# Kernel optimization log

Measured on AMD Instinct MI355X. Metric: run time of the kernel, lower is better.

Reference implementation:

```python
import jax, jax.numpy as jnp
import numpy as np

DIM = 512
HID = 1024
E = 8          # num_experts
K = 2          # num_experts_per_tok
B, S = 4, 2048


def setup_inputs() -> dict:
    key = jax.random.key(0)
    ks = jax.random.split(key, 10)
    sd = DIM ** -0.5
    sh = HID ** -0.5
    return {
        "x": jax.random.normal(ks[0], (B, S, DIM), dtype=jnp.float32),
        "gate_w": jax.random.normal(ks[1], (E, DIM), dtype=jnp.float32) * sd,
        "biases": jnp.zeros((E,), dtype=jnp.float32),  # e_expert_biases
        # routed experts: swiglu  y = (silu(x@w1) * (x@w3)) @ w2
        "w1": jax.random.normal(ks[2], (E, DIM, HID), dtype=jnp.float32) * sd,
        "w3": jax.random.normal(ks[3], (E, DIM, HID), dtype=jnp.float32) * sd,
        "w2": jax.random.normal(ks[4], (E, HID, DIM), dtype=jnp.float32) * sh,
        # single shared expert
        "sw1": jax.random.normal(ks[5], (DIM, HID), dtype=jnp.float32) * sd,
        "sw3": jax.random.normal(ks[6], (DIM, HID), dtype=jnp.float32) * sd,
        "sw2": jax.random.normal(ks[7], (HID, DIM), dtype=jnp.float32) * sh,
    }


def reference(x, gate_w, biases, w1, w3, w2, sw1, sw3, sw2):
    Bb, Ss, D = x.shape
    xt = x.reshape(Bb * Ss, D)                      # [T, D]

    # shared expert (applied to full x)
    shared = (jax.nn.silu(xt @ sw1) * (xt @ sw3)) @ sw2  # [T, D]

    # router
    scores = xt @ gate_w.T                          # [T, E]
    # indices chosen from biased scores (aux-free load balancing)
    _, idx = jax.lax.top_k(scores + biases, K)      # [T, K] int
    # gate values are top-k of the UNBIASED scores (as in original code)
    topv, _ = jax.lax.top_k(scores, K)              # [T, K]
    p = jax.nn.sigmoid(topv)
    p = p / jnp.sum(p, axis=-1, keepdims=True)      # [T, K]

    # every expert on every token (dense-combine MoE reference)
    h = jax.nn.silu(jnp.einsum('td,edh->eth', xt, w1)) * jnp.einsum('td,edh->eth', xt, w3)
    y = jnp.einsum('eth,ehd->etd', h, w2)           # [E, T, D]

    onehot = jax.nn.one_hot(idx, E, dtype=xt.dtype)  # [T, K, E]
    comb = jnp.einsum('tk,tke->te', p, onehot)       # [T, E] combine weights
    out = jnp.einsum('te,etd->td', comb, y) + shared
    return out.reshape(Bb, Ss, D)
```

## Files before the change

kernel.cpp:

```cpp
#include <hip/hip_runtime.h>
#include <hip/hip_bf16.h>


#define Tn 8192
#define Dd 512
#define Hh 1024
#define NEx 9

typedef __attribute__((ext_vector_type(8))) short short8;
typedef __attribute__((ext_vector_type(4))) float f32x4;

#define AS1 __attribute__((address_space(1)))
#define AS3 __attribute__((address_space(3)))

#define OFF_XB    ((size_t)0)
#define OFF_W13T  (OFF_XB + (size_t)Tn * Dd * 2)
#define OFF_W2T   (OFF_W13T + (size_t)NEx * 2 * Hh * Dd * 2)
#define OFF_HBUF  (OFF_W2T + (size_t)NEx * Dd * Hh * 2)
#define OFF_TOK   (OFF_HBUF + (size_t)(3 * Tn) * Hh * 2)
#define OFF_SLOTP (OFF_TOK + (size_t)8 * Tn * 4)
#define OFF_PG    (OFF_SLOTP + (size_t)Tn * 2 * 4)
#define OFF_CNT   (OFF_PG + (size_t)Tn * 2 * 4)
#define OFF_OFFS  (OFF_CNT + 1024)
#define OFF_YC    OFF_XB

__device__ __forceinline__ ushort f2bf(float f) {
    unsigned int u = __float_as_uint(f);
    return (ushort)((u + 0x7fffu + ((u >> 16) & 1u)) >> 16);
}
__device__ __forceinline__ float bf2f(short s) {
    return __uint_as_float(((unsigned int)(unsigned short)s) << 16);
}

__global__ __launch_bounds__(256) void trans_kernel(
        const float* __restrict__ w1, const float* __restrict__ sw1,
        const float* __restrict__ w3, const float* __restrict__ sw3,
        const float* __restrict__ w2, const float* __restrict__ sw2,
        ushort* __restrict__ w13t, ushort* __restrict__ w2t) {
    __shared__ float tile[32][33];
    int z = blockIdx.z;
    int fam = z / 9, sl = z - fam * 9;
    int tx = threadIdx.x & 31, ty = threadIdx.x >> 5;
    if (fam < 2) {
        const float* base = (fam == 0) ? ((sl < 8) ? w1 + (size_t)sl * Dd * Hh : sw1)
                                       : ((sl < 8) ? w3 + (size_t)sl * Dd * Hh : sw3);
        ushort* dst = w13t + (size_t)sl * 2 * Hh * Dd;
        int c0 = blockIdx.x * 32, r0 = blockIdx.y * 32;
#pragma unroll
        for (int k = 0; k < 4; ++k)
            tile[ty + 8 * k][tx] = base[(size_t)(r0 + ty + 8 * k) * Hh + c0 + tx];
        __syncthreads();
#pragma unroll
        for (int k = 0; k < 4; ++k) {
            int h = c0 + ty + 8 * k;
            int n = (((h >> 4) * 2 + fam) << 4) + (h & 15);
            dst[(size_t)n * Dd + r0 + tx] = f2bf(tile[tx][ty + 8 * k]);
        }
    } else {
        const float* base = (sl < 8) ? w2 + (size_t)sl * Dd * Hh : sw2;
        ushort* dst = w2t + (size_t)sl * Dd * Hh;
        int r0 = blockIdx.x * 32, c0 = blockIdx.y * 32;
#pragma unroll
        for (int k = 0; k < 4; ++k)
            tile[ty + 8 * k][tx] = base[(size_t)(r0 + ty + 8 * k) * Dd + c0 + tx];
        __syncthreads();
#pragma unroll
        for (int k = 0; k < 4; ++k)
            dst[(size_t)(c0 + ty + 8 * k) * Hh + r0 + tx] = f2bf(tile[tx][ty + 8 * k]);
    }
}

__global__ __launch_bounds__(256) void router_kernel(const float* __restrict__ x,
                                                     const float* __restrict__ gw,
                                                     const float* __restrict__ bias,
                                                     int* __restrict__ cnt,
                                                     int* __restrict__ tok,
                                                     int* __restrict__ slotp,
                                                     float* __restrict__ pg,
                                                     ushort* __restrict__ xb) {
    __shared__ int le[64];
    __shared__ float lg[64];
    __shared__ int lpos[64];
    __shared__ int lcnt[8];
    __shared__ int gbase[8];
    int tid = threadIdx.x, lane = tid & 63, wave = tid >> 6;
    if (tid < 8) lcnt[tid] = 0;
    __syncthreads();
    int t0 = blockIdx.x * 32 + wave * 8;
    for (int it = 0; it < 8; ++it) {
        int t = t0 + it;
        const float4* xr = (const float4*)(x + (size_t)t * Dd);
        float4 xa = xr[lane * 2], xc = xr[lane * 2 + 1];
        ushort4 o1, o2;
        o1.x = f2bf(xa.x); o1.y = f2bf(xa.y); o1.z = f2bf(xa.z); o1.w = f2bf(xa.w);
        o2.x = f2bf(xc.x); o2.y = f2bf(xc.y); o2.z = f2bf(xc.z); o2.w = f2bf(xc.w);
        *(ushort4*)(xb + (size_t)t * Dd + lane * 8) = o1;
        *(ushort4*)(xb + (size_t)t * Dd + lane * 8 + 4) = o2;
        float sc[8];
#pragma unroll
        for (int e = 0; e < 8; ++e) {
            const float4* gr = (const float4*)(gw + (size_t)e * Dd);
            float4 ga = gr[lane * 2], gc = gr[lane * 2 + 1];
            float s = xa.x * ga.x + xa.y * ga.y + xa.z * ga.z + xa.w * ga.w
                    + xc.x * gc.x + xc.y * gc.y + xc.z * gc.z + xc.w * gc.w;
#pragma unroll
            for (int o = 32; o > 0; o >>= 1) s += __shfl_xor(s, o);
            sc[e] = s;
        }
        if (lane == 0) {
            float b0 = -1e30f; int i0 = 0;
#pragma unroll
            for (int e = 0; e < 8; ++e) { float bv = sc[e] + bias[e]; if (bv > b0) { b0 = bv; i0 = e; } }
            float b1v = -1e30f; int i1 = (i0 == 0) ? 1 : 0;
#pragma unroll
            for (int e = 0; e < 8; ++e) if (e != i0) { float bv = sc[e] + bias[e]; if (bv > b1v) { b1v = bv; i1 = e; } }
            float v0 = -1e30f; int k0i = 0;
#pragma unroll
            for (int e = 0; e < 8; ++e) if (sc[e] > v0) { v0 = sc[e]; k0i = e; }
            float v1 = -1e30f;
#pragma unroll
            for (int e = 0; e < 8; ++e) if (e != k0i && sc[e] > v1) v1 = sc[e];
            float p0 = 1.f / (1.f + __expf(-v0));
            float p1 = 1.f / (1.f + __expf(-v1));
            float inv = 1.f / (p0 + p1);
            int ai = (wave * 8 + it) * 2;
            le[ai] = i0;     lg[ai] = p0 * inv;
            le[ai + 1] = i1; lg[ai + 1] = p1 * inv;
        }
    }
    __syncthreads();
    if (tid < 64) lpos[tid] = atomicAdd(&lcnt[le[tid]], 1);
    __syncthreads();
    if (tid < 8) gbase[tid] = atomicAdd(&cnt[tid * 32], lcnt[tid]);
    __syncthreads();
    if (tid < 64) {
        int e = le[tid];
        int dst = gbase[e] + lpos[tid];
        int t = blockIdx.x * 32 + (tid >> 1);
        tok[(size_t)e * Tn + dst] = t;
        slotp[t * 2 + (tid & 1)] = (e << 16) | dst;
        pg[t * 2 + (tid & 1)] = lg[tid];
    }
}

__global__ void scan_kernel(const int* cnt, int* off, int* cntc) {
    if (threadIdx.x == 0 && blockIdx.x == 0) {
        int s = 0;
        for (int e = 0; e < 8; ++e) { int c = cnt[e * 32]; cntc[e] = c; off[e] = s; s += c; }
        off[8] = s;
        cntc[8] = Tn;
    }
}

__global__ __launch_bounds__(256, 2) void stage1_kernel(
        const ushort* __restrict__ xb, const ushort* __restrict__ w13t,
        const int* __restrict__ tok, const int* __restrict__ cntc,
        const int* __restrict__ off, ushort* __restrict__ Hbuf) {
    int e = blockIdx.z;
    int cn = cntc[e];
    int m0 = blockIdx.x * 128;
    if (m0 >= cn) return;
    int n0 = blockIdx.y * 128;
    const ushort* we = w13t + (size_t)e * 2 * Hh * Dd;

    __shared__ ushort As[128 * 64];
    __shared__ ushort Bs[128 * 64];
    __shared__ int toks[128];

    int tid = threadIdx.x;
    if (tid < 128) {
        int slot = m0 + tid;
        int sl = slot < cn ? slot : cn - 1;
        toks[tid] = (e == 8) ? sl : tok[(size_t)e * Tn + sl];
    }
    __syncthreads();

    int lane = tid & 63, wave = tid >> 6;
    int wm = (wave & 1) * 64, wn = (wave >> 1) * 64;
    int col15 = lane & 15, quad = lane >> 4;
    int lr = lane >> 3;
    int lcx = ((lane & 7) ^ lr) * 8;

    f32x4 acc[4][4];
#pragma unroll
    for (int a = 0; a < 4; ++a)
#pragma unroll
        for (int b = 0; b < 4; ++b) acc[a][b] = (f32x4){0.f, 0.f, 0.f, 0.f};

    for (int kb = 0; kb < Dd; kb += 64) {
#pragma unroll
        for (int i = 0; i < 4; ++i) {
            int cid = wave * 4 + i;
            const ushort* g = xb + (size_t)toks[cid * 8 + lr] * Dd + kb + lcx;
            __builtin_amdgcn_global_load_lds((const AS1 void*)g, (AS3 void*)(As + cid * 512), 16, 0, 0);
        }
#pragma unroll
        for (int i = 0; i < 4; ++i) {
            int cid = wave * 4 + i;
            const ushort* g = we + (size_t)(n0 + cid * 8 + lr) * Dd + kb + lcx;
            __builtin_amdgcn_global_load_lds((const AS1 void*)g, (AS3 void*)(Bs + cid * 512), 16, 0, 0);
        }
        __syncthreads();
#pragma unroll
        for (int ks = 0; ks < 2; ++ks) {
            int px = ((ks * 4 + quad) ^ (col15 & 7)) * 8;
            short8 a[4], b[4];
#pragma unroll
            for (int mi = 0; mi < 4; ++mi)
                a[mi] = *(const short8*)&As[(wm + mi * 16 + col15) * 64 + px];
#pragma unroll
            for (int ni = 0; ni < 4; ++ni)
                b[ni] = *(const short8*)&Bs[(wn + ni * 16 + col15) * 64 + px];
#pragma unroll
            for (int mi = 0; mi < 4; ++mi)
#pragma unroll
                for (int ni = 0; ni < 4; ++ni)
                    acc[mi][ni] = __builtin_amdgcn_mfma_f32_16x16x32_bf16(a[mi], b[ni], acc[mi][ni], 0, 0, 0);
        }
        __syncthreads();
    }

    int oe = off[e];
    int hbase = (n0 + wn) >> 1;
#pragma unroll
    for (int mi = 0; mi < 4; ++mi)
#pragma unroll
        for (int r = 0; r < 4; ++r) {
            int slot = m0 + wm + mi * 16 + quad * 4 + r;
            if (slot < cn) {
                size_t rowb = (size_t)(oe + slot) * Hh;
#pragma unroll
                for (int np = 0; np < 2; ++np) {
                    float h1 = acc[mi][np * 2][r], h3 = acc[mi][np * 2 + 1][r];
                    float s = h1 / (1.f + __expf(-h1));
                    Hbuf[rowb + hbase + np * 16 + col15] = f2bf(s * h3);
                }
            }
        }
}

__global__ __launch_bounds__(256, 3) void stage2_kernel(
        const ushort* __restrict__ Hbuf, const ushort* __restrict__ w2t,
        const int* __restrict__ cntc, const int* __restrict__ off,
        ushort* __restrict__ Yc) {
    int e = blockIdx.z;
    int cn = cntc[e];
    int m0 = blockIdx.x * 128;
    if (m0 >= cn) return;
    int n0 = blockIdx.y * 128;
    int oe = off[e];
    const ushort* w2e = w2t + (size_t)e * Dd * Hh;

    __shared__ ushort As[128 * 64];
    __shared__ ushort Bs[128 * 64];

    int tid = threadIdx.x;
    int lane = tid & 63, wave = tid >> 6;
    int wm = (wave & 1) * 64, wn = (wave >> 1) * 64;
    int col15 = lane & 15, quad = lane >> 4;
    int lr = lane >> 3;
    int lcx = ((lane & 7) ^ lr) * 8;

    f32x4 acc[4][4];
#pragma unroll
    for (int a = 0; a < 4; ++a)
#pragma unroll
        for (int b = 0; b < 4; ++b) acc[a][b] = (f32x4){0.f, 0.f, 0.f, 0.f};

    for (int kb = 0; kb < Hh; kb += 64) {
#pragma unroll
        for (int i = 0; i < 4; ++i) {
            int cid = wave * 4 + i;
            const ushort* g = Hbuf + (size_t)(oe + m0 + cid * 8 + lr) * Hh + kb + lcx;
            __builtin_amdgcn_global_load_lds((const AS1 void*)g, (AS3 void*)(As + cid * 512), 16, 0, 0);
        }
#pragma unroll
        for (int i = 0; i < 4; ++i) {
            int cid = wave * 4 + i;
            const ushort* g = w2e + (size_t)(n0 + cid * 8 + lr) * Hh + kb + lcx;
            __builtin_amdgcn_global_load_lds((const AS1 void*)g, (AS3 void*)(Bs + cid * 512), 16, 0, 0);
        }
        __syncthreads();
#pragma unroll
        for (int ks = 0; ks < 2; ++ks) {
            int px = ((ks * 4 + quad) ^ (col15 & 7)) * 8;
            short8 a[4], b[4];
#pragma unroll
            for (int mi = 0; mi < 4; ++mi)
                a[mi] = *(const short8*)&As[(wm + mi * 16 + col15) * 64 + px];
#pragma unroll
            for (int ni = 0; ni < 4; ++ni)
                b[ni] = *(const short8*)&Bs[(wn + ni * 16 + col15) * 64 + px];
#pragma unroll
            for (int mi = 0; mi < 4; ++mi)
#pragma unroll
                for (int ni = 0; ni < 4; ++ni)
                    acc[mi][ni] = __builtin_amdgcn_mfma_f32_16x16x32_bf16(a[mi], b[ni], acc[mi][ni], 0, 0, 0);
        }
        __syncthreads();
    }

#pragma unroll
    for (int mi = 0; mi < 4; ++mi)
#pragma unroll
        for (int r = 0; r < 4; ++r) {
            int slot = m0 + wm + mi * 16 + quad * 4 + r;
            if (slot < cn) {
                size_t rowb = (size_t)(oe + slot) * Dd;
#pragma unroll
                for (int ni = 0; ni < 4; ++ni)
                    Yc[rowb + n0 + wn + ni * 16 + col15] = f2bf(acc[mi][ni][r]);
            }
        }
}

__global__ __launch_bounds__(256) void combine_kernel(const ushort* __restrict__ Yc,
        const int* __restrict__ slotp, const float* __restrict__ pg,
        const int* __restrict__ off, float* __restrict__ out) {
    int g = blockIdx.x * 256 + threadIdx.x;
    int t = g >> 6;
    int c = (g & 63) * 8;
    int p0 = slotp[t * 2], p1 = slotp[t * 2 + 1];
    float g0 = pg[t * 2], g1 = pg[t * 2 + 1];
    int s0 = off[p0 >> 16] + (p0 & 0xffff);
    int s1 = off[p1 >> 16] + (p1 & 0xffff);
    int s2 = off[8] + t;
    short8 a = *(const short8*)(Yc + (size_t)s0 * Dd + c);
    short8 b = *(const short8*)(Yc + (size_t)s1 * Dd + c);
    short8 d = *(const short8*)(Yc + (size_t)s2 * Dd + c);
    float o[8];
#pragma unroll
    for (int i = 0; i < 8; ++i)
        o[i] = g0 * bf2f(a[i]) + g1 * bf2f(b[i]) + bf2f(d[i]);
    float* dst = out + (size_t)t * Dd + c;
    *(float4*)dst = (float4){o[0], o[1], o[2], o[3]};
    *(float4*)(dst + 4) = (float4){o[4], o[5], o[6], o[7]};
}

extern "C" void kernel_launch(void* const* d_in, const int* in_sizes, int n_in,
                              void* d_out, int out_size, void* d_ws, size_t ws_size,
                              hipStream_t stream) {
    (void)in_sizes; (void)n_in; (void)out_size; (void)ws_size;
    const float* x    = (const float*)d_in[0];
    const float* gw   = (const float*)d_in[1];
    const float* bias = (const float*)d_in[2];
    const float* w1   = (const float*)d_in[3];
    const float* w3   = (const float*)d_in[4];
    const float* w2   = (const float*)d_in[5];
    const float* sw1  = (const float*)d_in[6];
    const float* sw3  = (const float*)d_in[7];
    const float* sw2  = (const float*)d_in[8];
    float* out = (float*)d_out;

    char* ws = (char*)d_ws;
    ushort* xb    = (ushort*)(ws + OFF_XB);
    ushort* w13t  = (ushort*)(ws + OFF_W13T);
    ushort* w2t   = (ushort*)(ws + OFF_W2T);
    ushort* Hbuf  = (ushort*)(ws + OFF_HBUF);
    ushort* Yc    = (ushort*)(ws + OFF_YC);
    int*    tok   = (int*)(ws + OFF_TOK);
    int*    slotp = (int*)(ws + OFF_SLOTP);
    float*  pg    = (float*)(ws + OFF_PG);
    int*    cnt   = (int*)(ws + OFF_CNT);
    int*    off   = (int*)(ws + OFF_OFFS);
    int*    cntc  = off + 16;

    hipMemsetAsync(cnt, 0, 1024, stream);

    trans_kernel<<<dim3(32, 16, 27), 256, 0, stream>>>(w1, sw1, w3, sw3, w2, sw2, w13t, w2t);
    router_kernel<<<256, 256, 0, stream>>>(x, gw, bias, cnt, tok, slotp, pg, xb);
    scan_kernel<<<1, 64, 0, stream>>>(cnt, off, cntc);

    stage1_kernel<<<dim3(64, 16, NEx), 256, 0, stream>>>(xb, w13t, tok, cntc, off, Hbuf);
    stage2_kernel<<<dim3(64, Dd / 128, NEx), 256, 0, stream>>>(Hbuf, w2t, cntc, off, Yc);
    combine_kernel<<<2048, 256, 0, stream>>>(Yc, slotp, pg, off, out);
}
```

Before: 264.1 us.

## Use 256x256 tiles with 8 waves and double-buffered ping-pong LDS pipeline

Replaces the 128x128, 4-wave grouped GEMM tiles in both expert stages with a shared 256x256 core using 8 waves and 128 KB of LDS in two stages. Async global-to-LDS loads are interleaved with MFMA quarter-blocks under explicit barriers, waitcnts and setprio. The goal is more data reuse per tile and hiding global load latency behind compute. In exchange, the larger tiles waste more work on partial expert tiles and launch fewer blocks, which could hurt occupancy and load balance.

```diff
diff --git a/kernel.cpp b/kernel.cpp
--- a/kernel.cpp
+++ b/kernel.cpp
@@ -152,81 +152,157 @@
     }
 }
 
-__global__ __launch_bounds__(256, 2) void stage1_kernel(
+__device__ __forceinline__ void mm256_core(
+        const ushort* (&aSrc)[2][2], const ushort* (&bSrc)[2][2],
+        ushort* smem, int KK, f32x4 (&acc)[8][4]) {
+    const int tid = threadIdx.x;
+    const int lane = tid & 63, wid = tid >> 6;
+    const int wm = wid >> 2, wn = wid & 3, hb = wn >> 1, wn1 = wn & 1;
+    const int col15 = lane & 15, quad = lane >> 4, sw7 = col15 & 7;
+
+    ushort* Ard = smem + wm * 8192;
+    ushort* Brd = smem + 32768 + hb * 8192;
+    ushort* Adst = smem + wid * 1024;
+    ushort* Bdst = smem + 32768 + wid * 1024;
+
+    auto rdA = [&](int s, int mi, int ks) -> short8 {
+        return *(const short8*)&Ard[s * 16384 + mi * 1024 + col15 * 64 + (((ks * 4 + quad) ^ sw7) << 3)];
+    };
+    auto rdB = [&](int s, int ni, int ks) -> short8 {
+        return *(const short8*)&Brd[s * 16384 + (wn1 * 64 + ni * 16 + col15) * 64 + (((ks * 4 + quad) ^ sw7) << 3)];
+    };
+    auto stA = [&](int s, int h, int kb) {
+        if (kb < KK) {
+            __builtin_amdgcn_global_load_lds((const AS1 void*)(aSrc[h][0] + kb), (AS3 void*)(Adst + (s * 2 + h) * 8192), 16, 0, 0);
+            __builtin_amdgcn_global_load_lds((const AS1 void*)(aSrc[h][1] + kb), (AS3 void*)(Adst + (s * 2 + h) * 8192 + 512), 16, 0, 0);
+        }
+    };
+    auto stB = [&](int s, int h, int kb) {
+        if (kb < KK) {
+            __builtin_amdgcn_global_load_lds((const AS1 void*)(bSrc[h][0] + kb), (AS3 void*)(Bdst + (s * 2 + h) * 8192), 16, 0, 0);
+            __builtin_amdgcn_global_load_lds((const AS1 void*)(bSrc[h][1] + kb), (AS3 void*)(Bdst + (s * 2 + h) * 8192 + 512), 16, 0, 0);
+        }
+    };
+
+    short8 aF[4][2], bF0[2][2], bF1[2][2];
+    auto ldA = [&](int s, int mh) {
+#pragma unroll
+        for (int j = 0; j < 4; ++j) { aF[j][0] = rdA(s, mh * 4 + j, 0); aF[j][1] = rdA(s, mh * 4 + j, 1); }
+    };
+    auto ldB = [&](int s, int nh, short8 (&bF)[2][2]) {
+#pragma unroll
+        for (int t = 0; t < 2; ++t) { bF[t][0] = rdB(s, nh * 2 + t, 0); bF[t][1] = rdB(s, nh * 2 + t, 1); }
+    };
+    auto mmq = [&](int mh, int nh, short8 (&bF)[2][2]) {
+        __builtin_amdgcn_s_setprio(1);
+#pragma unroll
+        for (int j = 0; j < 4; ++j)
+#pragma unroll
+            for (int t = 0; t < 2; ++t) {
+                acc[mh * 4 + j][nh * 2 + t] = __builtin_amdgcn_mfma_f32_16x16x32_bf16(aF[j][0], bF[t][0], acc[mh * 4 + j][nh * 2 + t], 0, 0, 0);
+                acc[mh * 4 + j][nh * 2 + t] = __builtin_amdgcn_mfma_f32_16x16x32_bf16(aF[j][1], bF[t][1], acc[mh * 4 + j][nh * 2 + t], 0, 0, 0);
+            }
+        __builtin_amdgcn_s_setprio(0);
+    };
+
+#define BAR()  __builtin_amdgcn_s_barrier()
+#define LGK0() do { asm volatile("s_waitcnt lgkmcnt(0)" ::: "memory"); __builtin_amdgcn_sched_barrier(0); } while (0)
+
+    stA(0, 0, 0); stB(0, 0, 0); stB(0, 1, 0); stA(0, 1, 0);
+    stA(1, 0, 64); stB(1, 0, 64);
+    asm volatile("s_waitcnt vmcnt(4)" ::: "memory");
+    BAR();
+
+    const int NIT = KK >> 7;
+    for (int i = 0; i < NIT; ++i) {
+        const int k0 = i << 7;
+        const bool tail = (i == NIT - 1);
+        ldA(0, 0); ldB(0, 0, bF0);
+        stA(1, 1, k0 + 64);
+        BAR(); LGK0(); mmq(0, 0, bF0); BAR();
+        ldB(0, 1, bF1);
+        stB(1, 1, k0 + 64);
+        BAR(); LGK0(); mmq(0, 1, bF1); BAR();
+        ldA(0, 1);
+        stA(0, 0, k0 + 128);
+        BAR(); LGK0(); mmq(1, 0, bF0); BAR();
+        stB(0, 0, k0 + 128);
+        BAR(); mmq(1, 1, bF1);
+        if (tail) asm volatile("s_waitcnt vmcnt(0)" ::: "memory");
+        else      asm volatile("s_waitcnt vmcnt(4)" ::: "memory");
+        BAR();
+        ldA(1, 0); ldB(1, 0, bF0);
+        stB(0, 1, k0 + 128);
+        BAR(); LGK0(); mmq(0, 0, bF0); BAR();
+        ldB(1, 1, bF1);
+        stA(0, 1, k0 + 128);
+        BAR(); LGK0(); mmq(0, 1, bF1); BAR();
+        ldA(1, 1);
+        stA(1, 0, k0 + 192);
+        BAR(); LGK0(); mmq(1, 0, bF0); BAR();
+        stB(1, 0, k0 + 192);
+        BAR(); mmq(1, 1, bF1);
+        if (tail) asm volatile("s_waitcnt vmcnt(0)" ::: "memory");
+        else      asm volatile("s_waitcnt vmcnt(4)" ::: "memory");
+        BAR();
+    }
+#undef BAR
+#undef LGK0
+}
+
+__global__ __launch_bounds__(512, 2) void stage1_kernel(
         const ushort* __restrict__ xb, const ushort* __restrict__ w13t,
         const int* __restrict__ tok, const int* __restrict__ cntc,
         const int* __restrict__ off, ushort* __restrict__ Hbuf) {
+    __shared__ __align__(16) ushort smem[65536];
+    __shared__ int toks[256];
     int e = blockIdx.z;
     int cn = cntc[e];
-    int m0 = blockIdx.x * 128;
+    int m0 = blockIdx.x * 256;
     if (m0 >= cn) return;
-    int n0 = blockIdx.y * 128;
+    int n0 = blockIdx.y * 256;
     const ushort* we = w13t + (size_t)e * 2 * Hh * Dd;
 
-    __shared__ ushort As[128 * 64];
-    __shared__ ushort Bs[128 * 64];
-    __shared__ int toks[128];
-
     int tid = threadIdx.x;
-    if (tid < 128) {
+    if (tid < 256) {
         int slot = m0 + tid;
         int sl = slot < cn ? slot : cn - 1;
         toks[tid] = (e == 8) ? sl : tok[(size_t)e * Tn + sl];
     }
     __syncthreads();
 
-    int lane = tid & 63, wave = tid >> 6;
-    int wm = (wave & 1) * 64, wn = (wave >> 1) * 64;
+    int lane = tid & 63, wid = tid >> 6;
+    int lr = lane >> 3, l7 = lane & 7;
+    int lcx = (l7 ^ lr) << 3;
+
+    const ushort* aSrc[2][2];
+    const ushort* bSrc[2][2];
+#pragma unroll
+    for (int h = 0; h < 2; ++h)
+#pragma unroll
+        for (int r = 0; r < 2; ++r) {
+            int row = h * 128 + wid * 16 + r * 8 + lr;
+            aSrc[h][r] = xb + (size_t)toks[row] * Dd + lcx;
+            bSrc[h][r] = we + (size_t)(n0 + row) * Dd + lcx;
+        }
+
+    f32x4 acc[8][4];
+#pragma unroll
+    for (int a = 0; a < 8; ++a)
+#pragma unroll
+        for (int b = 0; b < 4; ++b) acc[a][b] = (f32x4){0.f, 0.f, 0.f, 0.f};
+
+    mm256_core(aSrc, bSrc, smem, Dd, acc);
+
+    int wm = wid >> 2, wn = wid & 3;
     int col15 = lane & 15, quad = lane >> 4;
-    int lr = lane >> 3;
-    int lcx = ((lane & 7) ^ lr) * 8;
-
-    f32x4 acc[4][4];
-#pragma unroll
-    for (int a = 0; a < 4; ++a)
-#pragma unroll
-        for (int b = 0; b < 4; ++b) acc[a][b] = (f32x4){0.f, 0.f, 0.f, 0.f};
-
-    for (int kb = 0; kb < Dd; kb += 64) {
-#pragma unroll
-        for (int i = 0; i < 4; ++i) {
-            int cid = wave * 4 + i;
-            const ushort* g = xb + (size_t)toks[cid * 8 + lr] * Dd + kb + lcx;
-            __builtin_amdgcn_global_load_lds((const AS1 void*)g, (AS3 void*)(As + cid * 512), 16, 0, 0);
-        }
-#pragma unroll
-        for (int i = 0; i < 4; ++i) {
-            int cid = wave * 4 + i;
-            const ushort* g = we + (size_t)(n0 + cid * 8 + lr) * Dd + kb + lcx;
-            __builtin_amdgcn_global_load_lds((const AS1 void*)g, (AS3 void*)(Bs + cid * 512), 16, 0, 0);
-        }
-        __syncthreads();
-#pragma unroll
-        for (int ks = 0; ks < 2; ++ks) {
-            int px = ((ks * 4 + quad) ^ (col15 & 7)) * 8;
-            short8 a[4], b[4];
-#pragma unroll
-            for (int mi = 0; mi < 4; ++mi)
-                a[mi] = *(const short8*)&As[(wm + mi * 16 + col15) * 64 + px];
-#pragma unroll
-            for (int ni = 0; ni < 4; ++ni)
-                b[ni] = *(const short8*)&Bs[(wn + ni * 16 + col15) * 64 + px];
-#pragma unroll
-            for (int mi = 0; mi < 4; ++mi)
-#pragma unroll
-                for (int ni = 0; ni < 4; ++ni)
-                    acc[mi][ni] = __builtin_amdgcn_mfma_f32_16x16x32_bf16(a[mi], b[ni], acc[mi][ni], 0, 0, 0);
-        }
-        __syncthreads();
-    }
-
     int oe = off[e];
-    int hbase = (n0 + wn) >> 1;
-#pragma unroll
-    for (int mi = 0; mi < 4; ++mi)
+    int hbase = (n0 >> 1) + wn * 32;
+#pragma unroll
+    for (int mi = 0; mi < 8; ++mi)
 #pragma unroll
         for (int r = 0; r < 4; ++r) {
-            int slot = m0 + wm + mi * 16 + quad * 4 + r;
+            int slot = m0 + wm * 128 + mi * 16 + quad * 4 + r;
             if (slot < cn) {
                 size_t rowb = (size_t)(oe + slot) * Hh;
 #pragma unroll
@@ -239,77 +315,55 @@
         }
 }
 
-__global__ __launch_bounds__(256, 3) void stage2_kernel(
+__global__ __launch_bounds__(512, 2) void stage2_kernel(
         const ushort* __restrict__ Hbuf, const ushort* __restrict__ w2t,
         const int* __restrict__ cntc, const int* __restrict__ off,
         ushort* __restrict__ Yc) {
+    __shared__ __align__(16) ushort smem[65536];
     int e = blockIdx.z;
     int cn = cntc[e];
-    int m0 = blockIdx.x * 128;
+    int m0 = blockIdx.x * 256;
     if (m0 >= cn) return;
-    int n0 = blockIdx.y * 128;
+    int n0 = blockIdx.y * 256;
     int oe = off[e];
     const ushort* w2e = w2t + (size_t)e * Dd * Hh;
 
-    __shared__ ushort As[128 * 64];
-    __shared__ ushort Bs[128 * 64];
-
     int tid = threadIdx.x;
-    int lane = tid & 63, wave = tid >> 6;
-    int wm = (wave & 1) * 64, wn = (wave >> 1) * 64;
+    int lane = tid & 63, wid = tid >> 6;
+    int lr = lane >> 3, l7 = lane & 7;
+    int lcx = (l7 ^ lr) << 3;
+
+    const ushort* aSrc[2][2];
+    const ushort* bSrc[2][2];
+#pragma unroll
+    for (int h = 0; h < 2; ++h)
+#pragma unroll
+        for (int r = 0; r < 2; ++r) {
+            int row = h * 128 + wid * 16 + r * 8 + lr;
+            aSrc[h][r] = Hbuf + (size_t)(oe + m0 + row) * Hh + lcx;
+            bSrc[h][r] = w2e + (size_t)(n0 + row) * Hh + lcx;
+        }
+
+    f32x4 acc[8][4];
+#pragma unroll
+    for (int a = 0; a < 8; ++a)
+#pragma unroll
+        for (int b = 0; b < 4; ++b) acc[a][b] = (f32x4){0.f, 0.f, 0.f, 0.f};
+
+    mm256_core(aSrc, bSrc, smem, Hh, acc);
+
+    int wm = wid >> 2, wn = wid & 3;
     int col15 = lane & 15, quad = lane >> 4;
-    int lr = lane >> 3;
-    int lcx = ((lane & 7) ^ lr) * 8;
-
-    f32x4 acc[4][4];
-#pragma unroll
-    for (int a = 0; a < 4; ++a)
-#pragma unroll
-        for (int b = 0; b < 4; ++b) acc[a][b] = (f32x4){0.f, 0.f, 0.f, 0.f};
-
-    for (int kb = 0; kb < Hh; kb += 64) {
-#pragma unroll
-        for (int i = 0; i < 4; ++i) {
-            int cid = wave * 4 + i;
-            const ushort* g = Hbuf + (size_t)(oe + m0 + cid * 8 + lr) * Hh + kb + lcx;
-            __builtin_amdgcn_global_load_lds((const AS1 void*)g, (AS3 void*)(As + cid * 512), 16, 0, 0);
-        }
-#pragma unroll
-        for (int i = 0; i < 4; ++i) {
-            int cid = wave * 4 + i;
-            const ushort* g = w2e + (size_t)(n0 + cid * 8 + lr) * Hh + kb + lcx;
-            __builtin_amdgcn_global_load_lds((const AS1 void*)g, (AS3 void*)(Bs + cid * 512), 16, 0, 0);
-        }
-        __syncthreads();
-#pragma unroll
-        for (int ks = 0; ks < 2; ++ks) {
-            int px = ((ks * 4 + quad) ^ (col15 & 7)) * 8;
-            short8 a[4], b[4];
-#pragma unroll
-            for (int mi = 0; mi < 4; ++mi)
-                a[mi] = *(const short8*)&As[(wm + mi * 16 + col15) * 64 + px];
-#pragma unroll
-            for (int ni = 0; ni < 4; ++ni)
-                b[ni] = *(const short8*)&Bs[(wn + ni * 16 + col15) * 64 + px];
-#pragma unroll
-            for (int mi = 0; mi < 4; ++mi)
-#pragma unroll
-                for (int ni = 0; ni < 4; ++ni)
-                    acc[mi][ni] = __builtin_amdgcn_mfma_f32_16x16x32_bf16(a[mi], b[ni], acc[mi][ni], 0, 0, 0);
-        }
-        __syncthreads();
-    }
-
-#pragma unroll
-    for (int mi = 0; mi < 4; ++mi)
+#pragma unroll
+    for (int mi = 0; mi < 8; ++mi)
 #pragma unroll
         for (int r = 0; r < 4; ++r) {
-            int slot = m0 + wm + mi * 16 + quad * 4 + r;
+            int slot = m0 + wm * 128 + mi * 16 + quad * 4 + r;
             if (slot < cn) {
                 size_t rowb = (size_t)(oe + slot) * Dd;
 #pragma unroll
                 for (int ni = 0; ni < 4; ++ni)
-                    Yc[rowb + n0 + wn + ni * 16 + col15] = f2bf(acc[mi][ni][r]);
+                    Yc[rowb + n0 + wn * 64 + ni * 16 + col15] = f2bf(acc[mi][ni][r]);
             }
         }
 }
@@ -371,7 +425,7 @@
     router_kernel<<<256, 256, 0, stream>>>(x, gw, bias, cnt, tok, slotp, pg, xb);
     scan_kernel<<<1, 64, 0, stream>>>(cnt, off, cntc);
 
-    stage1_kernel<<<dim3(64, 16, NEx), 256, 0, stream>>>(xb, w13t, tok, cntc, off, Hbuf);
-    stage2_kernel<<<dim3(64, Dd / 128, NEx), 256, 0, stream>>>(Hbuf, w2t, cntc, off, Yc);
+    stage1_kernel<<<dim3(32, 8, NEx), 512, 0, stream>>>(xb, w13t, tok, cntc, off, Hbuf);
+    stage2_kernel<<<dim3(32, Dd / 256, NEx), 512, 0, stream>>>(Hbuf, w2t, cntc, off, Yc);
     combine_kernel<<<2048, 256, 0, stream>>>(Yc, slotp, pg, off, out);
 }
```

New measurement: 390.4 us. +47.8%, slower.

## Double-buffer LDS tiles in both expert GEMM stages to overlap loads

Applied to the files above, without the earlier changes.

Both grouped GEMM kernels now keep two LDS buffers for the A and B tiles. The global-to-LDS loads for the next K-slice are issued before the MFMA work on the current slice, so load latency can overlap with compute instead of stalling at a barrier every iteration. This doubles shared memory per block to about 64 KB, and stage2's occupancy hint drops from 3 to 2 blocks per CU. There is a possible ordering risk: the only barrier per iteration sits after the MFMAs, with no explicit wait that the prefetched async LDS loads have landed before the buffer is read in the next iteration.

```diff
diff --git a/kernel.cpp b/kernel.cpp
--- a/kernel.cpp
+++ b/kernel.cpp
@@ -163,8 +163,8 @@
     int n0 = blockIdx.y * 128;
     const ushort* we = w13t + (size_t)e * 2 * Hh * Dd;
 
-    __shared__ ushort As[128 * 64];
-    __shared__ ushort Bs[128 * 64];
+    __shared__ ushort As[2][128 * 64];
+    __shared__ ushort Bs[2][128 * 64];
     __shared__ int toks[128];
 
     int tid = threadIdx.x;
@@ -187,30 +187,36 @@
 #pragma unroll
         for (int b = 0; b < 4; ++b) acc[a][b] = (f32x4){0.f, 0.f, 0.f, 0.f};
 
-    for (int kb = 0; kb < Dd; kb += 64) {
+    auto stage = [&](int buf, int kb) {
 #pragma unroll
         for (int i = 0; i < 4; ++i) {
             int cid = wave * 4 + i;
             const ushort* g = xb + (size_t)toks[cid * 8 + lr] * Dd + kb + lcx;
-            __builtin_amdgcn_global_load_lds((const AS1 void*)g, (AS3 void*)(As + cid * 512), 16, 0, 0);
+            __builtin_amdgcn_global_load_lds((const AS1 void*)g, (AS3 void*)(&As[buf][cid * 512]), 16, 0, 0);
         }
 #pragma unroll
         for (int i = 0; i < 4; ++i) {
             int cid = wave * 4 + i;
             const ushort* g = we + (size_t)(n0 + cid * 8 + lr) * Dd + kb + lcx;
-            __builtin_amdgcn_global_load_lds((const AS1 void*)g, (AS3 void*)(Bs + cid * 512), 16, 0, 0);
-        }
-        __syncthreads();
+            __builtin_amdgcn_global_load_lds((const AS1 void*)g, (AS3 void*)(&Bs[buf][cid * 512]), 16, 0, 0);
+        }
+    };
+
+    stage(0, 0);
+    __syncthreads();
+    int cur = 0;
+    for (int kb = 0; kb < Dd; kb += 64) {
+        if (kb + 64 < Dd) stage(cur ^ 1, kb + 64);
 #pragma unroll
         for (int ks = 0; ks < 2; ++ks) {
             int px = ((ks * 4 + quad) ^ (col15 & 7)) * 8;
             short8 a[4], b[4];
 #pragma unroll
             for (int mi = 0; mi < 4; ++mi)
-                a[mi] = *(const short8*)&As[(wm + mi * 16 + col15) * 64 + px];
+                a[mi] = *(const short8*)&As[cur][(wm + mi * 16 + col15) * 64 + px];
 #pragma unroll
             for (int ni = 0; ni < 4; ++ni)
-                b[ni] = *(const short8*)&Bs[(wn + ni * 16 + col15) * 64 + px];
+                b[ni] = *(const short8*)&Bs[cur][(wn + ni * 16 + col15) * 64 + px];
 #pragma unroll
             for (int mi = 0; mi < 4; ++mi)
 #pragma unroll
@@ -218,6 +224,7 @@
                     acc[mi][ni] = __builtin_amdgcn_mfma_f32_16x16x32_bf16(a[mi], b[ni], acc[mi][ni], 0, 0, 0);
         }
         __syncthreads();
+        cur ^= 1;
     }
 
     int oe = off[e];
@@ -239,7 +246,7 @@
         }
 }
 
-__global__ __launch_bounds__(256, 3) void stage2_kernel(
+__global__ __launch_bounds__(256, 2) void stage2_kernel(
         const ushort* __restrict__ Hbuf, const ushort* __restrict__ w2t,
         const int* __restrict__ cntc, const int* __restrict__ off,
         ushort* __restrict__ Yc) {
@@ -251,8 +258,8 @@
     int oe = off[e];
     const ushort* w2e = w2t + (size_t)e * Dd * Hh;
 
-    __shared__ ushort As[128 * 64];
-    __shared__ ushort Bs[128 * 64];
+    __shared__ ushort As[2][128 * 64];
+    __shared__ ushort Bs[2][128 * 64];
 
     int tid = threadIdx.x;
     int lane = tid & 63, wave = tid >> 6;
@@ -267,30 +274,36 @@
 #pragma unroll
         for (int b = 0; b < 4; ++b) acc[a][b] = (f32x4){0.f, 0.f, 0.f, 0.f};
 
-    for (int kb = 0; kb < Hh; kb += 64) {
+    auto stage = [&](int buf, int kb) {
 #pragma unroll
         for (int i = 0; i < 4; ++i) {
             int cid = wave * 4 + i;
             const ushort* g = Hbuf + (size_t)(oe + m0 + cid * 8 + lr) * Hh + kb + lcx;
-            __builtin_amdgcn_global_load_lds((const AS1 void*)g, (AS3 void*)(As + cid * 512), 16, 0, 0);
+            __builtin_amdgcn_global_load_lds((const AS1 void*)g, (AS3 void*)(&As[buf][cid * 512]), 16, 0, 0);
         }
 #pragma unroll
         for (int i = 0; i < 4; ++i) {
             int cid = wave * 4 + i;
             const ushort* g = w2e + (size_t)(n0 + cid * 8 + lr) * Hh + kb + lcx;
-            __builtin_amdgcn_global_load_lds((const AS1 void*)g, (AS3 void*)(Bs + cid * 512), 16, 0, 0);
-        }
-        __syncthreads();
+            __builtin_amdgcn_global_load_lds((const AS1 void*)g, (AS3 void*)(&Bs[buf][cid * 512]), 16, 0, 0);
+        }
+    };
+
+    stage(0, 0);
+    __syncthreads();
+    int cur = 0;
+    for (int kb = 0; kb < Hh; kb += 64) {
+        if (kb + 64 < Hh) stage(cur ^ 1, kb + 64);
 #pragma unroll
         for (int ks = 0; ks < 2; ++ks) {
             int px = ((ks * 4 + quad) ^ (col15 & 7)) * 8;
             short8 a[4], b[4];
 #pragma unroll
             for (int mi = 0; mi < 4; ++mi)
-                a[mi] = *(const short8*)&As[(wm + mi * 16 + col15) * 64 + px];
+                a[mi] = *(const short8*)&As[cur][(wm + mi * 16 + col15) * 64 + px];
 #pragma unroll
             for (int ni = 0; ni < 4; ++ni)
-                b[ni] = *(const short8*)&Bs[(wn + ni * 16 + col15) * 64 + px];
+                b[ni] = *(const short8*)&Bs[cur][(wn + ni * 16 + col15) * 64 + px];
 #pragma unroll
             for (int mi = 0; mi < 4; ++mi)
 #pragma unroll
@@ -298,6 +311,7 @@
                     acc[mi][ni] = __builtin_amdgcn_mfma_f32_16x16x32_bf16(a[mi], b[ni], acc[mi][ni], 0, 0, 0);
         }
         __syncthreads();
+        cur ^= 1;
     }
 
 #pragma unroll
```

Measured after the change: 332.4 us. +25.8%, slower.
